# Performance work log

Measured on AMD Instinct MI355X. Metric: run time of the kernel, lower is better.

Reference implementation:

```python
import jax, jax.numpy as jnp
import numpy as np

L = 4      # number of Verifier layers in the linked list
D = 1536   # constraint matrix dimension


def setup_inputs() -> dict:
    key = jax.random.key(0)
    ks = jax.random.split(key, 6)
    scale = 0.02  # keep chained matmul magnitudes sane
    lb = jax.random.normal(ks[0], (1, D), jnp.float32)
    ub = lb + jax.random.uniform(ks[1], (1, D), jnp.float32)  # ensure lb <= ub
    lcs = scale * jax.random.normal(ks[2], (L, D, D), jnp.float32)
    ucs = lcs + scale * jax.random.uniform(ks[3], (L, D, D), jnp.float32)
    lc_bias = jax.random.normal(ks[4], (L, D), jnp.float32)
    uc_bias = lc_bias + jax.random.uniform(ks[5], (L, D), jnp.float32)
    return {"lb": lb, "ub": ub, "lcs": lcs, "ucs": ucs,
            "lc_bias": lc_bias, "uc_bias": uc_bias}


def reference(lb, ub, lcs, ucs, lc_bias, uc_bias):
    pos = lambda x: jnp.maximum(x, 0.0)
    neg = lambda x: jnp.minimum(x, 0.0)
    n_layers = lcs.shape[0]

    # Layer 0 forward: its backsubstitution returns these bounds unchanged
    # (prev is None), and all later backsubs terminate on these stored bounds.
    lb0 = lb @ pos(lcs[0]).T + ub @ neg(lcs[0]).T + lc_bias[0]
    ub0 = ub @ pos(ucs[0]).T + lb @ neg(ucs[0]).T + uc_bias[0]
    cur_lb, cur_ub = lb0, ub0

    for k in range(1, n_layers):
        # backsubstitution from layer k: start with transposed constraint
        C_lc, C_uc = lcs[k].T, ucs[k].T           # [D, D]
        C_lcb, C_ucb = lc_bias[k], uc_bias[k]     # [D]
        # recurse through layers k-1 .. 0, combining constraints
        for j in range(k - 1, -1, -1):
            pU, nU = pos(C_uc), neg(C_uc)
            pL, nL = pos(C_lc), neg(C_lc)
            new_ucb = uc_bias[j] @ pU + lc_bias[j] @ nU + C_ucb
            new_uc = ucs[j].T @ pU + lcs[j].T @ nU
            new_lcb = lc_bias[j] @ pL + uc_bias[j] @ nL + C_lcb
            new_lc = lcs[j].T @ pL + ucs[j].T @ nL
            C_lc, C_uc, C_lcb, C_ucb = new_lc, new_uc, new_lcb, new_ucb
        # apply combined constraint to layer-0 stored bounds
        cur_lb = lb0 @ pos(C_lc) + ub0 @ neg(C_lc) + C_lcb
        cur_ub = ub0 @ pos(C_uc) + lb0 @ neg(C_uc) + C_ucb

    return cur_lb, cur_ub
```

## Files before the change

### kernel.cpp

```cpp
#include <hip/hip_runtime.h>

#define D 1536
#define BT 96
#define BK 64
#define NT (D / BK)
#define TT 64

typedef unsigned short u16;
typedef short bf16x8 __attribute__((ext_vector_type(8)));
typedef short short2v __attribute__((ext_vector_type(2)));
typedef float f32x4 __attribute__((ext_vector_type(4)));

static __device__ __forceinline__ float bf2f(u16 s) {
    unsigned u = ((unsigned)s) << 16;
    float f; __builtin_memcpy(&f, &u, 4); return f;
}
static __device__ __forceinline__ u16 f2bf(float f) {
    unsigned u; __builtin_memcpy(&u, &f, 4);
    unsigned r = (u + 0x7FFFu + ((u >> 16) & 1u)) >> 16;
    return (u16)r;
}

static __device__ __forceinline__ void splitpn(bf16x8 a, bf16x8& p, bf16x8& n) {
    union U { bf16x8 v; short2v s[4]; unsigned u[4]; } x, up, un;
    x.v = a;
#pragma unroll
    for (int i = 0; i < 4; ++i) {
        short2v m = x.s[i] >> 15;
        unsigned mu; __builtin_memcpy(&mu, &m, 4);
        unsigned ng = x.u[i] & mu;
        un.u[i] = ng;
        up.u[i] = x.u[i] ^ ng;
    }
    p = up.v; n = un.v;
}

#define GLDS(g, s) __builtin_amdgcn_global_load_lds( \
    (const __attribute__((address_space(1))) void*)(g), \
    (__attribute__((address_space(3))) void*)(s), 16, 0, 0)

__global__ __launch_bounds__(256) void prep_k(
    const float* __restrict__ lcs, const float* __restrict__ ucs,
    u16* __restrict__ lcsT, u16* __restrict__ ucsT,
    u16* __restrict__ Ga, u16* __restrict__ Gc)
{
    const int z = blockIdx.z;
    const int r0 = blockIdx.y * TT, c0 = blockIdx.x * TT;
    const int tid = threadIdx.x;

    if (z >= 6) {
        const float* src = (z == 6 ? ucs : lcs) + (size_t)3 * D * D;
        u16* dst = (z == 6) ? Ga : Gc;
#pragma unroll
        for (int i = 0; i < 2; ++i) {
            int r = (tid >> 3) + i * 32, cc = (tid & 7) * 8;
            const float* p = src + (size_t)(r0 + r) * D + c0 + cc;
            f32x4 x0 = *(const f32x4*)p;
            f32x4 x1 = *(const f32x4*)(p + 4);
            bf16x8 y;
#pragma unroll
            for (int e = 0; e < 4; ++e) { y[e] = (short)f2bf(x0[e]); y[e + 4] = (short)f2bf(x1[e]); }
            *(bf16x8*)(dst + (size_t)(r0 + r) * D + c0 + cc) = y;
        }
        return;
    }

    __shared__ u16 t[TT][TT + 8];
    const int j = z >> 1, sel = z & 1;
    const float* src = (sel ? ucs : lcs) + (size_t)j * D * D;
    u16* dst = (sel ? ucsT : lcsT) + (size_t)j * D * D;
#pragma unroll
    for (int i = 0; i < 2; ++i) {
        int c = tid + i * 256; int r = c >> 3, v = c & 7;
        const float* p = src + (size_t)(r0 + r) * D + c0 + v * 8;
        f32x4 x0 = *(const f32x4*)p;
        f32x4 x1 = *(const f32x4*)(p + 4);
        bf16x8 y;
#pragma unroll
        for (int e = 0; e < 4; ++e) { y[e] = (short)f2bf(x0[e]); y[e + 4] = (short)f2bf(x1[e]); }
        *(bf16x8*)&t[r][v * 8] = y;
    }
    __syncthreads();
#pragma unroll
    for (int i = 0; i < 2; ++i) {
        int c = tid + i * 256; int rr = c >> 3, v = c & 7;
        bf16x8 x;
#pragma unroll
        for (int e = 0; e < 8; ++e) x[e] = (short)t[v * 8 + e][rr];
        *(bf16x8*)(dst + (size_t)(c0 + rr) * D + r0 + v * 8) = x;
    }
}

__global__ __launch_bounds__(256) void vec_k(
    const float* __restrict__ lb, const float* __restrict__ ub,
    const float* __restrict__ lcs, const float* __restrict__ ucs,
    const float* __restrict__ lcb, const float* __restrict__ ucb,
    float* __restrict__ lb0, float* __restrict__ ub0,
    float* __restrict__ cb_uc, float* __restrict__ cb_lc)
{
    const int tt = blockIdx.x * 4 + (threadIdx.x >> 6);
    const int lane = threadIdx.x & 63;
    const int kind = tt >> 10;
    const int n = tt & 1535;
    const int which = tt / D;
    const int row_n = tt - which * D;

    const float* row; const float* vp; const float* vn;
    if (which == 0)      { row = lcs + (size_t)row_n * D;               vp = lb;           vn = ub; }
    else if (which == 1) { row = ucs + (size_t)row_n * D;               vp = ub;           vn = lb; }
    else if (which == 2) { row = ucs + (size_t)(3 * (size_t)D * D) + (size_t)row_n * D; vp = ucb + 2 * D; vn = lcb + 2 * D; }
    else                 { row = lcs + (size_t)(3 * (size_t)D * D) + (size_t)row_n * D; vp = lcb + 2 * D; vn = ucb + 2 * D; }

    float s = 0.f;
    for (int c2 = 0; c2 < D / 256; ++c2) {
        int base = (c2 * 64 + lane) * 4;
        f32x4 g = *(const f32x4*)(row + base);
        f32x4 p = *(const f32x4*)(vp + base);
        f32x4 m = *(const f32x4*)(vn + base);
#pragma unroll
        for (int e = 0; e < 4; ++e) s += g[e] * (g[e] > 0.f ? p[e] : m[e]);
    }
#pragma unroll
    for (int o = 32; o; o >>= 1) s += __shfl_down(s, o);
    if (lane == 0) {
        if (which == 0)      lb0[row_n] = s + lcb[row_n];
        else if (which == 1) ub0[row_n] = s + ucb[row_n];
        else if (which == 2) cb_uc[row_n] = s + ucb[3 * D + row_n];
        else                 cb_lc[row_n] = s + lcb[3 * D + row_n];
    }
    (void)kind; (void)n;
}

struct GemmArgs { };

static __device__ __forceinline__ void stage_tile(
    const u16* __restrict__ A, const u16* __restrict__ Bp, const u16* __restrict__ Bn,
    int r0, int c0, int kt, u16* __restrict__ sbuf, int tid, int wid)
{
#pragma unroll
    for (int i = 0; i < 9; ++i) {
        const int idx = (i % 3) * 256 + tid;
        const int row = idx >> 3;
        const int kc = tid & 7;
        const int kcg = kc ^ (row & 7);
        const u16* base = (i < 3) ? (A + (size_t)(r0 + row) * D)
                        : ((i < 6) ? (Bp + (size_t)(c0 + row) * D)
                                   : (Bn + (size_t)(c0 + row) * D));
        GLDS(base + kt + kcg * 8, (char*)sbuf + (i * 256 + wid * 64) * 16);
    }
}

static __device__ __forceinline__ void compute_tile(
    const u16* __restrict__ sbuf, f32x4 (&acc)[3][3], int mb, int nb, int lrow, int lk)
{
#pragma unroll
    for (int ks = 0; ks < 2; ++ks) {
        const int slot = ks * 4 + lk;
        bf16x8 pa[3], na[3];
#pragma unroll
        for (int mi = 0; mi < 3; ++mi) {
            int row = mb + mi * 16 + lrow;
            int x = slot ^ (row & 7);
            bf16x8 a = *(const bf16x8*)(sbuf + row * BK + x * 8);
            splitpn(a, pa[mi], na[mi]);
        }
#pragma unroll
        for (int ni = 0; ni < 3; ++ni) {
            int row = nb + ni * 16 + lrow;
            int x = slot ^ (row & 7);
            bf16x8 bu = *(const bf16x8*)(sbuf + BT * BK + row * BK + x * 8);
            bf16x8 bl = *(const bf16x8*)(sbuf + 2 * BT * BK + row * BK + x * 8);
#pragma unroll
            for (int mi = 0; mi < 3; ++mi) {
                acc[mi][ni] = __builtin_amdgcn_mfma_f32_16x16x32_bf16(pa[mi], bu, acc[mi][ni], 0, 0, 0);
                acc[mi][ni] = __builtin_amdgcn_mfma_f32_16x16x32_bf16(na[mi], bl, acc[mi][ni], 0, 0, 0);
            }
        }
    }
}

__global__ __launch_bounds__(256, 2) void gemm_step(
    const u16* __restrict__ Guc, const u16* __restrict__ Glc,
    const u16* __restrict__ lcsTj, const u16* __restrict__ ucsTj,
    u16* __restrict__ outU, u16* __restrict__ outL,
    const float* __restrict__ ucbN, const float* __restrict__ lcbN,
    float* __restrict__ cb_uc, float* __restrict__ cb_lc)
{
    __shared__ u16 smemA[3 * BT * BK];
    __shared__ u16 smemB[3 * BT * BK];
    const int chain = blockIdx.z;
    const u16* A  = chain ? Glc : Guc;
    const u16* Bp = chain ? lcsTj : ucsTj;
    const u16* Bn = chain ? ucsTj : lcsTj;
    u16* out = chain ? outL : outU;
    const int r0 = blockIdx.y * BT, c0 = blockIdx.x * BT;
    const int tid = threadIdx.x, lane = tid & 63, wid = tid >> 6;
    const int mb = (wid >> 1) * 48, nb = (wid & 1) * 48;
    const int lrow = lane & 15, lk = lane >> 4;

    f32x4 acc[3][3] = {};

    stage_tile(A, Bp, Bn, r0, c0, 0, smemA, tid, wid);
    asm volatile("s_waitcnt vmcnt(0)" ::: "memory");
    __syncthreads();

#pragma unroll 1
    for (int t2 = 0; t2 < NT / 2; ++t2) {
        const int t = t2 * 2;
        stage_tile(A, Bp, Bn, r0, c0, (t + 1) * BK, smemB, tid, wid);
        compute_tile(smemA, acc, mb, nb, lrow, lk);
        __syncthreads();
        if (t2 < NT / 2 - 1)
            stage_tile(A, Bp, Bn, r0, c0, (t + 2) * BK, smemA, tid, wid);
        compute_tile(smemB, acc, mb, nb, lrow, lk);
        __syncthreads();
    }

    if (ucbN) {
        const float* pb_ = chain ? lcbN : ucbN;
        const float* nb_ = chain ? ucbN : lcbN;
        float* cb = chain ? cb_lc : cb_uc;
        float pbv[3], nbv[3];
#pragma unroll
        for (int ni = 0; ni < 3; ++ni) {
            int c = c0 + nb + ni * 16 + lrow;
            pbv[ni] = pb_[c]; nbv[ni] = nb_[c];
        }
#pragma unroll
        for (int mi = 0; mi < 3; ++mi)
#pragma unroll
            for (int q = 0; q < 4; ++q) {
                float s = 0.f;
#pragma unroll
                for (int ni = 0; ni < 3; ++ni) {
                    float g = acc[mi][ni][q];
                    s += g * (g > 0.f ? pbv[ni] : nbv[ni]);
                }
                s += __shfl_xor(s, 1); s += __shfl_xor(s, 2);
                s += __shfl_xor(s, 4); s += __shfl_xor(s, 8);
                if (lrow == 0)
                    atomicAdd(&cb[r0 + mb + mi * 16 + lk * 4 + q], s);
            }
    }

#pragma unroll
    for (int mi = 0; mi < 3; ++mi)
#pragma unroll
        for (int ni = 0; ni < 3; ++ni) {
            int c = c0 + nb + ni * 16 + lrow;
            int rbase = r0 + mb + mi * 16 + lk * 4;
#pragma unroll
            for (int q = 0; q < 4; ++q)
                out[(size_t)(rbase + q) * D + c] = f2bf(acc[mi][ni][q]);
        }
}

__global__ __launch_bounds__(256) void final_k(
    const u16* __restrict__ Guc, const u16* __restrict__ Glc,
    const float* __restrict__ cb_uc, const float* __restrict__ cb_lc,
    const float* __restrict__ lb0, const float* __restrict__ ub0,
    float* __restrict__ out)
{
    const int gw = blockIdx.x * 4 + (threadIdx.x >> 6);
    const int lane = threadIdx.x & 63;
    const int which = gw >= D;
    const int n = which ? gw - D : gw;
    const u16* row = (which ? Guc : Glc) + (size_t)n * D;
    const float* vp = which ? ub0 : lb0;
    const float* vn = which ? lb0 : ub0;
    float s = 0.f;
    for (int c2 = 0; c2 < D / 512; ++c2) {
        int base = (c2 * 64 + lane) * 8;
        bf16x8 g8 = *(const bf16x8*)(row + base);
        f32x4 p0 = *(const f32x4*)(vp + base);
        f32x4 p1 = *(const f32x4*)(vp + base + 4);
        f32x4 n0 = *(const f32x4*)(vn + base);
        f32x4 n1 = *(const f32x4*)(vn + base + 4);
#pragma unroll
        for (int e = 0; e < 8; ++e) {
            float g = bf2f((u16)g8[e]);
            float pv = e < 4 ? p0[e] : p1[e - 4];
            float nv = e < 4 ? n0[e] : n1[e - 4];
            s += g * (g > 0.f ? pv : nv);
        }
    }
#pragma unroll
    for (int o = 32; o; o >>= 1) s += __shfl_down(s, o);
    if (lane == 0) {
        float b = (which ? cb_uc : cb_lc)[n];
        out[which * D + n] = s + b;
    }
}

extern "C" void kernel_launch(void* const* d_in, const int* in_sizes, int n_in,
                              void* d_out, int out_size, void* d_ws, size_t ws_size,
                              hipStream_t stream) {
    const float* lb  = (const float*)d_in[0];
    const float* ub  = (const float*)d_in[1];
    const float* lcs = (const float*)d_in[2];
    const float* ucs = (const float*)d_in[3];
    const float* lcb = (const float*)d_in[4];
    const float* ucb = (const float*)d_in[5];
    float* out = (float*)d_out;

    const size_t DD = (size_t)D * D;
    u16* ws   = (u16*)d_ws;
    u16* lcsT = ws;
    u16* ucsT = lcsT + 3 * DD;
    u16* Ga = ucsT + 3 * DD;
    u16* Gb = Ga + DD;
    u16* Gc = Gb + DD;
    u16* Gd = Gc + DD;
    float* fbuf  = (float*)(Gd + DD);
    float* lb0   = fbuf;
    float* ub0   = fbuf + D;
    float* cb_uc = fbuf + 2 * D;
    float* cb_lc = fbuf + 3 * D;

    prep_k<<<dim3(D / TT, D / TT, 8), 256, 0, stream>>>(lcs, ucs, lcsT, ucsT, Ga, Gc);
    vec_k<<<dim3(4 * D / 4), 256, 0, stream>>>(lb, ub, lcs, ucs, lcb, ucb, lb0, ub0, cb_uc, cb_lc);

    u16* curU = Ga; u16* curL = Gc;
    u16* altU = Gb; u16* altL = Gd;
    for (int j = 2; j >= 0; --j) {
        const float* ucbN = (j > 0) ? (ucb + (size_t)(j - 1) * D) : nullptr;
        const float* lcbN = (j > 0) ? (lcb + (size_t)(j - 1) * D) : nullptr;
        gemm_step<<<dim3(D / BT, D / BT, 2), 256, 0, stream>>>(
            curU, curL, lcsT + (size_t)j * DD, ucsT + (size_t)j * DD, altU, altL,
            ucbN, lcbN, cb_uc, cb_lc);
        u16* t;
        t = curU; curU = altU; altU = t;
        t = curL; curL = altL; altL = t;
    }
    final_k<<<dim3(2 * D / 4), 256, 0, stream>>>(curU, curL, cb_uc, cb_lc, lb0, ub0, out);
}
```

Baseline: 134.2 us.

## Fuse upper/lower chains in one GEMM block with triple-buffered LDS pipeline

Each block now computes both the upper and lower constraint chains for the same output tile, so the B tiles (ucsT, lcsT) are loaded once and shared by both chains instead of once per chain via blockIdx.z. The k-loop changes from double buffering to a three-stage ring with explicit vmcnt waits and raw barriers, prefetching two tiles ahead. The cost is half as many blocks (256 instead of 512), twice the accumulators per thread and 144 KB of LDS with occupancy dropped to one block per CU, which may leave some CUs idle or underutilised.

```diff
diff --git a/kernel.cpp b/kernel.cpp
--- a/kernel.cpp
+++ b/kernel.cpp
@@ -5,6 +5,8 @@
 #define BK 64
 #define NT (D / BK)
 #define TT 64
+#define TILE_E (BT * BK)
+#define BUF_E (4 * TILE_E)
 
 typedef unsigned short u16;
 typedef short bf16x8 __attribute__((ext_vector_type(8)));
@@ -39,6 +41,8 @@
     (const __attribute__((address_space(1))) void*)(g), \
     (__attribute__((address_space(3))) void*)(s), 16, 0, 0)
 
+#define MFMA16(a, b, c) __builtin_amdgcn_mfma_f32_16x16x32_bf16(a, b, c, 0, 0, 0)
+
 __global__ __launch_bounds__(256) void prep_k(
     const float* __restrict__ lcs, const float* __restrict__ ucs,
     u16* __restrict__ lcsT, u16* __restrict__ ucsT,
@@ -100,8 +104,6 @@
 {
     const int tt = blockIdx.x * 4 + (threadIdx.x >> 6);
     const int lane = threadIdx.x & 63;
-    const int kind = tt >> 10;
-    const int n = tt & 1535;
     const int which = tt / D;
     const int row_n = tt - which * D;
 
@@ -128,118 +130,126 @@
         else if (which == 2) cb_uc[row_n] = s + ucb[3 * D + row_n];
         else                 cb_lc[row_n] = s + lcb[3 * D + row_n];
     }
-    (void)kind; (void)n;
-}
-
-struct GemmArgs { };
+}
+
 
 static __device__ __forceinline__ void stage_tile(
-    const u16* __restrict__ A, const u16* __restrict__ Bp, const u16* __restrict__ Bn,
+    const u16* __restrict__ Au, const u16* __restrict__ Al,
+    const u16* __restrict__ Bu, const u16* __restrict__ Bl,
     int r0, int c0, int kt, u16* __restrict__ sbuf, int tid, int wid)
 {
 #pragma unroll
-    for (int i = 0; i < 9; ++i) {
+    for (int i = 0; i < 12; ++i) {
         const int idx = (i % 3) * 256 + tid;
         const int row = idx >> 3;
-        const int kc = tid & 7;
-        const int kcg = kc ^ (row & 7);
-        const u16* base = (i < 3) ? (A + (size_t)(r0 + row) * D)
-                        : ((i < 6) ? (Bp + (size_t)(c0 + row) * D)
-                                   : (Bn + (size_t)(c0 + row) * D));
-        GLDS(base + kt + kcg * 8, (char*)sbuf + (i * 256 + wid * 64) * 16);
+        const int kcg = (tid & 7) ^ (row & 7);
+        const u16* base; int ro;
+        if (i < 3)      { base = Au; ro = r0; }
+        else if (i < 6) { base = Al; ro = r0; }
+        else if (i < 9) { base = Bu; ro = c0; }
+        else            { base = Bl; ro = c0; }
+        GLDS(base + (size_t)(ro + row) * D + kt + kcg * 8,
+             (char*)sbuf + (i * 256 + wid * 64) * 16);
     }
 }
 
 static __device__ __forceinline__ void compute_tile(
-    const u16* __restrict__ sbuf, f32x4 (&acc)[3][3], int mb, int nb, int lrow, int lk)
+    const u16* __restrict__ sbuf, f32x4 (&accU)[3][3], f32x4 (&accL)[3][3],
+    int mb, int nb, int lrow, int lk)
 {
 #pragma unroll
     for (int ks = 0; ks < 2; ++ks) {
         const int slot = ks * 4 + lk;
-        bf16x8 pa[3], na[3];
+        bf16x8 pu[3], nu[3], pl[3], nl[3];
 #pragma unroll
         for (int mi = 0; mi < 3; ++mi) {
             int row = mb + mi * 16 + lrow;
             int x = slot ^ (row & 7);
-            bf16x8 a = *(const bf16x8*)(sbuf + row * BK + x * 8);
-            splitpn(a, pa[mi], na[mi]);
+            bf16x8 au = *(const bf16x8*)(sbuf + row * BK + x * 8);
+            bf16x8 al = *(const bf16x8*)(sbuf + TILE_E + row * BK + x * 8);
+            splitpn(au, pu[mi], nu[mi]);
+            splitpn(al, pl[mi], nl[mi]);
         }
 #pragma unroll
         for (int ni = 0; ni < 3; ++ni) {
             int row = nb + ni * 16 + lrow;
             int x = slot ^ (row & 7);
-            bf16x8 bu = *(const bf16x8*)(sbuf + BT * BK + row * BK + x * 8);
-            bf16x8 bl = *(const bf16x8*)(sbuf + 2 * BT * BK + row * BK + x * 8);
+            bf16x8 bu = *(const bf16x8*)(sbuf + 2 * TILE_E + row * BK + x * 8);
+            bf16x8 bl = *(const bf16x8*)(sbuf + 3 * TILE_E + row * BK + x * 8);
 #pragma unroll
             for (int mi = 0; mi < 3; ++mi) {
-                acc[mi][ni] = __builtin_amdgcn_mfma_f32_16x16x32_bf16(pa[mi], bu, acc[mi][ni], 0, 0, 0);
-                acc[mi][ni] = __builtin_amdgcn_mfma_f32_16x16x32_bf16(na[mi], bl, acc[mi][ni], 0, 0, 0);
+                accU[mi][ni] = MFMA16(pu[mi], bu, accU[mi][ni]);
+                accU[mi][ni] = MFMA16(nu[mi], bl, accU[mi][ni]);
+                accL[mi][ni] = MFMA16(pl[mi], bl, accL[mi][ni]);
+                accL[mi][ni] = MFMA16(nl[mi], bu, accL[mi][ni]);
             }
         }
     }
 }
 
-__global__ __launch_bounds__(256, 2) void gemm_step(
+__global__ __launch_bounds__(256, 1) void gemm_step(
     const u16* __restrict__ Guc, const u16* __restrict__ Glc,
     const u16* __restrict__ lcsTj, const u16* __restrict__ ucsTj,
     u16* __restrict__ outU, u16* __restrict__ outL,
     const float* __restrict__ ucbN, const float* __restrict__ lcbN,
     float* __restrict__ cb_uc, float* __restrict__ cb_lc)
 {
-    __shared__ u16 smemA[3 * BT * BK];
-    __shared__ u16 smemB[3 * BT * BK];
-    const int chain = blockIdx.z;
-    const u16* A  = chain ? Glc : Guc;
-    const u16* Bp = chain ? lcsTj : ucsTj;
-    const u16* Bn = chain ? ucsTj : lcsTj;
-    u16* out = chain ? outL : outU;
+    __shared__ u16 smem[3 * BUF_E];
     const int r0 = blockIdx.y * BT, c0 = blockIdx.x * BT;
     const int tid = threadIdx.x, lane = tid & 63, wid = tid >> 6;
     const int mb = (wid >> 1) * 48, nb = (wid & 1) * 48;
     const int lrow = lane & 15, lk = lane >> 4;
 
-    f32x4 acc[3][3] = {};
-
-    stage_tile(A, Bp, Bn, r0, c0, 0, smemA, tid, wid);
-    asm volatile("s_waitcnt vmcnt(0)" ::: "memory");
-    __syncthreads();
+    f32x4 accU[3][3] = {}, accL[3][3] = {};
+
+    stage_tile(Guc, Glc, ucsTj, lcsTj, r0, c0, 0, smem, tid, wid);
+    stage_tile(Guc, Glc, ucsTj, lcsTj, r0, c0, BK, smem + BUF_E, tid, wid);
 
 #pragma unroll 1
-    for (int t2 = 0; t2 < NT / 2; ++t2) {
-        const int t = t2 * 2;
-        stage_tile(A, Bp, Bn, r0, c0, (t + 1) * BK, smemB, tid, wid);
-        compute_tile(smemA, acc, mb, nb, lrow, lk);
-        __syncthreads();
-        if (t2 < NT / 2 - 1)
-            stage_tile(A, Bp, Bn, r0, c0, (t + 2) * BK, smemA, tid, wid);
-        compute_tile(smemB, acc, mb, nb, lrow, lk);
-        __syncthreads();
+    for (int t = 0; t < NT; ++t) {
+        if (t + 2 < NT) {
+            stage_tile(Guc, Glc, ucsTj, lcsTj, r0, c0, (t + 2) * BK,
+                       smem + ((t + 2) % 3) * BUF_E, tid, wid);
+            asm volatile("s_waitcnt vmcnt(24)" ::: "memory");
+        } else if (t + 2 == NT) {
+            asm volatile("s_waitcnt vmcnt(12)" ::: "memory");
+        } else {
+            asm volatile("s_waitcnt vmcnt(0)" ::: "memory");
+        }
+        __builtin_amdgcn_s_barrier();
+        compute_tile(smem + (t % 3) * BUF_E, accU, accL, mb, nb, lrow, lk);
+        asm volatile("" ::: "memory");
+        __builtin_amdgcn_s_barrier();
     }
 
     if (ucbN) {
-        const float* pb_ = chain ? lcbN : ucbN;
-        const float* nb_ = chain ? ucbN : lcbN;
-        float* cb = chain ? cb_lc : cb_uc;
-        float pbv[3], nbv[3];
+        float ubv[3], lbv[3];
 #pragma unroll
         for (int ni = 0; ni < 3; ++ni) {
             int c = c0 + nb + ni * 16 + lrow;
-            pbv[ni] = pb_[c]; nbv[ni] = nb_[c];
+            ubv[ni] = ucbN[c]; lbv[ni] = lcbN[c];
         }
 #pragma unroll
         for (int mi = 0; mi < 3; ++mi)
 #pragma unroll
             for (int q = 0; q < 4; ++q) {
-                float s = 0.f;
+                float sU = 0.f, sL = 0.f;
 #pragma unroll
                 for (int ni = 0; ni < 3; ++ni) {
-                    float g = acc[mi][ni][q];
-                    s += g * (g > 0.f ? pbv[ni] : nbv[ni]);
+                    float gU = accU[mi][ni][q];
+                    float gL = accL[mi][ni][q];
+                    sU += gU * (gU > 0.f ? ubv[ni] : lbv[ni]);
+                    sL += gL * (gL > 0.f ? lbv[ni] : ubv[ni]);
                 }
-                s += __shfl_xor(s, 1); s += __shfl_xor(s, 2);
-                s += __shfl_xor(s, 4); s += __shfl_xor(s, 8);
-                if (lrow == 0)
-                    atomicAdd(&cb[r0 + mb + mi * 16 + lk * 4 + q], s);
+                sU += __shfl_xor(sU, 1); sU += __shfl_xor(sU, 2);
+                sU += __shfl_xor(sU, 4); sU += __shfl_xor(sU, 8);
+                sL += __shfl_xor(sL, 1); sL += __shfl_xor(sL, 2);
+                sL += __shfl_xor(sL, 4); sL += __shfl_xor(sL, 8);
+                if (lrow == 0) {
+                    int r = r0 + mb + mi * 16 + lk * 4 + q;
+                    atomicAdd(&cb_uc[r], sU);
+                    atomicAdd(&cb_lc[r], sL);
+                }
             }
     }
 
@@ -250,8 +260,10 @@
             int c = c0 + nb + ni * 16 + lrow;
             int rbase = r0 + mb + mi * 16 + lk * 4;
 #pragma unroll
-            for (int q = 0; q < 4; ++q)
-                out[(size_t)(rbase + q) * D + c] = f2bf(acc[mi][ni][q]);
+            for (int q = 0; q < 4; ++q) {
+                outU[(size_t)(rbase + q) * D + c] = f2bf(accU[mi][ni][q]);
+                outL[(size_t)(rbase + q) * D + c] = f2bf(accL[mi][ni][q]);
+            }
         }
 }
 
@@ -325,7 +337,7 @@
     for (int j = 2; j >= 0; --j) {
         const float* ucbN = (j > 0) ? (ucb + (size_t)(j - 1) * D) : nullptr;
         const float* lcbN = (j > 0) ? (lcb + (size_t)(j - 1) * D) : nullptr;
-        gemm_step<<<dim3(D / BT, D / BT, 2), 256, 0, stream>>>(
+        gemm_step<<<dim3(D / BT, D / BT), 256, 0, stream>>>(
             curU, curL, lcsT + (size_t)j * DD, ucsT + (size_t)j * DD, altU, altL,
             ucbN, lcbN, cb_uc, cb_lc);
         u16* t;
```

Result: slower. 155.1 us (+15.6%).

## Use sum/difference B matrices with abs-sign A operand and deeper GEMM pipelining

Applied to the files above, without the earlier changes.

Replaces the positive/negative split of the A operand with an algebraic identity. The transposed ucs/lcs are preprocessed into half-sum and half-difference matrices, so each MFMA pair uses A as-is and |A| (sign-flipped for the lower chain) instead of masking into pos/neg parts. This cuts per-tile VALU splitting work and folds the chain-dependent B swap into a sign constant. The GEMM loop is also restructured to keep two tiles in flight with partial vmcnt waits and raw s_barrier, which aims for better overlap of loads and compute. The bf16 rounding of the (u±l)/2 values may change numerics slightly.

```diff
diff --git a/kernel.cpp b/kernel.cpp
--- a/kernel.cpp
+++ b/kernel.cpp
@@ -5,89 +5,91 @@
 #define BK 64
 #define NT (D / BK)
 #define TT 64
+#define TILE_E (BT * BK)
+#define BUF_E (3 * TILE_E)
 
 typedef unsigned short u16;
 typedef short bf16x8 __attribute__((ext_vector_type(8)));
-typedef short short2v __attribute__((ext_vector_type(2)));
 typedef float f32x4 __attribute__((ext_vector_type(4)));
 
-static __device__ __forceinline__ float bf2f(u16 s) {
-    unsigned u = ((unsigned)s) << 16;
-    float f; __builtin_memcpy(&f, &u, 4); return f;
-}
 static __device__ __forceinline__ u16 f2bf(float f) {
     unsigned u; __builtin_memcpy(&u, &f, 4);
     unsigned r = (u + 0x7FFFu + ((u >> 16) & 1u)) >> 16;
     return (u16)r;
 }
-
-static __device__ __forceinline__ void splitpn(bf16x8 a, bf16x8& p, bf16x8& n) {
-    union U { bf16x8 v; short2v s[4]; unsigned u[4]; } x, up, un;
-    x.v = a;
-#pragma unroll
-    for (int i = 0; i < 4; ++i) {
-        short2v m = x.s[i] >> 15;
-        unsigned mu; __builtin_memcpy(&mu, &m, 4);
-        unsigned ng = x.u[i] & mu;
-        un.u[i] = ng;
-        up.u[i] = x.u[i] ^ ng;
-    }
-    p = up.v; n = un.v;
+static __device__ __forceinline__ float bf2f(u16 s) {
+    unsigned u = ((unsigned)s) << 16;
+    float f; __builtin_memcpy(&f, &u, 4); return f;
 }
 
 #define GLDS(g, s) __builtin_amdgcn_global_load_lds( \
     (const __attribute__((address_space(1))) void*)(g), \
     (__attribute__((address_space(3))) void*)(s), 16, 0, 0)
 
+#define MFMA16(a, b, c) __builtin_amdgcn_mfma_f32_16x16x32_bf16(a, b, c, 0, 0, 0)
+
 __global__ __launch_bounds__(256) void prep_k(
     const float* __restrict__ lcs, const float* __restrict__ ucs,
-    u16* __restrict__ lcsT, u16* __restrict__ ucsT,
+    u16* __restrict__ BsT, u16* __restrict__ BdT,
     u16* __restrict__ Ga, u16* __restrict__ Gc)
 {
     const int z = blockIdx.z;
     const int r0 = blockIdx.y * TT, c0 = blockIdx.x * TT;
     const int tid = threadIdx.x;
 
-    if (z >= 6) {
-        const float* src = (z == 6 ? ucs : lcs) + (size_t)3 * D * D;
-        u16* dst = (z == 6) ? Ga : Gc;
-#pragma unroll
-        for (int i = 0; i < 2; ++i) {
-            int r = (tid >> 3) + i * 32, cc = (tid & 7) * 8;
-            const float* p = src + (size_t)(r0 + r) * D + c0 + cc;
-            f32x4 x0 = *(const f32x4*)p;
-            f32x4 x1 = *(const f32x4*)(p + 4);
-            bf16x8 y;
-#pragma unroll
-            for (int e = 0; e < 4; ++e) { y[e] = (short)f2bf(x0[e]); y[e + 4] = (short)f2bf(x1[e]); }
-            *(bf16x8*)(dst + (size_t)(r0 + r) * D + c0 + cc) = y;
+    if (z == 3) {
+#pragma unroll
+        for (int m = 0; m < 2; ++m) {
+            const float* src = (m ? lcs : ucs) + (size_t)3 * D * D;
+            u16* dst = m ? Gc : Ga;
+#pragma unroll
+            for (int i = 0; i < 2; ++i) {
+                int r = (tid >> 3) + i * 32, cc = (tid & 7) * 8;
+                const float* p = src + (size_t)(r0 + r) * D + c0 + cc;
+                f32x4 x0 = *(const f32x4*)p;
+                f32x4 x1 = *(const f32x4*)(p + 4);
+                bf16x8 y;
+#pragma unroll
+                for (int e = 0; e < 4; ++e) { y[e] = (short)f2bf(x0[e]); y[e + 4] = (short)f2bf(x1[e]); }
+                *(bf16x8*)(dst + (size_t)(r0 + r) * D + c0 + cc) = y;
+            }
         }
         return;
     }
 
-    __shared__ u16 t[TT][TT + 8];
-    const int j = z >> 1, sel = z & 1;
-    const float* src = (sel ? ucs : lcs) + (size_t)j * D * D;
-    u16* dst = (sel ? ucsT : lcsT) + (size_t)j * D * D;
+    __shared__ u16 ts[TT][TT + 8];
+    __shared__ u16 td[TT][TT + 8];
+    const float* srcl = lcs + (size_t)z * D * D;
+    const float* srcu = ucs + (size_t)z * D * D;
 #pragma unroll
     for (int i = 0; i < 2; ++i) {
         int c = tid + i * 256; int r = c >> 3, v = c & 7;
-        const float* p = src + (size_t)(r0 + r) * D + c0 + v * 8;
-        f32x4 x0 = *(const f32x4*)p;
-        f32x4 x1 = *(const f32x4*)(p + 4);
-        bf16x8 y;
-#pragma unroll
-        for (int e = 0; e < 4; ++e) { y[e] = (short)f2bf(x0[e]); y[e + 4] = (short)f2bf(x1[e]); }
-        *(bf16x8*)&t[r][v * 8] = y;
+        size_t off = (size_t)(r0 + r) * D + c0 + v * 8;
+        f32x4 l0 = *(const f32x4*)(srcl + off);
+        f32x4 l1 = *(const f32x4*)(srcl + off + 4);
+        f32x4 u0 = *(const f32x4*)(srcu + off);
+        f32x4 u1 = *(const f32x4*)(srcu + off + 4);
+        bf16x8 ys, yd;
+#pragma unroll
+        for (int e = 0; e < 4; ++e) {
+            ys[e]     = (short)f2bf((u0[e] + l0[e]) * 0.5f);
+            yd[e]     = (short)f2bf((u0[e] - l0[e]) * 0.5f);
+            ys[e + 4] = (short)f2bf((u1[e] + l1[e]) * 0.5f);
+            yd[e + 4] = (short)f2bf((u1[e] - l1[e]) * 0.5f);
+        }
+        *(bf16x8*)&ts[r][v * 8] = ys;
+        *(bf16x8*)&td[r][v * 8] = yd;
     }
     __syncthreads();
 #pragma unroll
     for (int i = 0; i < 2; ++i) {
         int c = tid + i * 256; int rr = c >> 3, v = c & 7;
-        bf16x8 x;
-#pragma unroll
-        for (int e = 0; e < 8; ++e) x[e] = (short)t[v * 8 + e][rr];
-        *(bf16x8*)(dst + (size_t)(c0 + rr) * D + r0 + v * 8) = x;
+        bf16x8 xs, xd;
+#pragma unroll
+        for (int e = 0; e < 8; ++e) { xs[e] = (short)ts[v * 8 + e][rr]; xd[e] = (short)td[v * 8 + e][rr]; }
+        size_t off = (size_t)z * D * D + (size_t)(c0 + rr) * D + r0 + v * 8;
+        *(bf16x8*)(BsT + off) = xs;
+        *(bf16x8*)(BdT + off) = xd;
     }
 }
 
@@ -100,8 +102,6 @@
 {
     const int tt = blockIdx.x * 4 + (threadIdx.x >> 6);
     const int lane = threadIdx.x & 63;
-    const int kind = tt >> 10;
-    const int n = tt & 1535;
     const int which = tt / D;
     const int row_n = tt - which * D;
 
@@ -128,52 +128,54 @@
         else if (which == 2) cb_uc[row_n] = s + ucb[3 * D + row_n];
         else                 cb_lc[row_n] = s + lcb[3 * D + row_n];
     }
-    (void)kind; (void)n;
-}
-
-struct GemmArgs { };
+}
+
 
 static __device__ __forceinline__ void stage_tile(
-    const u16* __restrict__ A, const u16* __restrict__ Bp, const u16* __restrict__ Bn,
+    const u16* __restrict__ A, const u16* __restrict__ Bs, const u16* __restrict__ Bd,
     int r0, int c0, int kt, u16* __restrict__ sbuf, int tid, int wid)
 {
 #pragma unroll
     for (int i = 0; i < 9; ++i) {
         const int idx = (i % 3) * 256 + tid;
         const int row = idx >> 3;
-        const int kc = tid & 7;
-        const int kcg = kc ^ (row & 7);
+        const int kcg = (tid & 7) ^ (row & 7);
         const u16* base = (i < 3) ? (A + (size_t)(r0 + row) * D)
-                        : ((i < 6) ? (Bp + (size_t)(c0 + row) * D)
-                                   : (Bn + (size_t)(c0 + row) * D));
+                        : ((i < 6) ? (Bs + (size_t)(c0 + row) * D)
+                                   : (Bd + (size_t)(c0 + row) * D));
         GLDS(base + kt + kcg * 8, (char*)sbuf + (i * 256 + wid * 64) * 16);
     }
 }
 
 static __device__ __forceinline__ void compute_tile(
-    const u16* __restrict__ sbuf, f32x4 (&acc)[3][3], int mb, int nb, int lrow, int lk)
+    const u16* __restrict__ sbuf, f32x4 (&acc)[3][3], unsigned sgn,
+    int mb, int nb, int lrow, int lk)
 {
 #pragma unroll
     for (int ks = 0; ks < 2; ++ks) {
         const int slot = ks * 4 + lk;
-        bf16x8 pa[3], na[3];
+        bf16x8 a[3], x[3];
 #pragma unroll
         for (int mi = 0; mi < 3; ++mi) {
             int row = mb + mi * 16 + lrow;
-            int x = slot ^ (row & 7);
-            bf16x8 a = *(const bf16x8*)(sbuf + row * BK + x * 8);
-            splitpn(a, pa[mi], na[mi]);
+            int xx = slot ^ (row & 7);
+            a[mi] = *(const bf16x8*)(sbuf + row * BK + xx * 8);
+            union { bf16x8 v; unsigned u[4]; } t, o;
+            t.v = a[mi];
+#pragma unroll
+            for (int q = 0; q < 4; ++q) o.u[q] = (t.u[q] & 0x7FFF7FFFu) ^ sgn;
+            x[mi] = o.v;
         }
 #pragma unroll
         for (int ni = 0; ni < 3; ++ni) {
             int row = nb + ni * 16 + lrow;
-            int x = slot ^ (row & 7);
-            bf16x8 bu = *(const bf16x8*)(sbuf + BT * BK + row * BK + x * 8);
-            bf16x8 bl = *(const bf16x8*)(sbuf + 2 * BT * BK + row * BK + x * 8);
+            int xx = slot ^ (row & 7);
+            bf16x8 bs = *(const bf16x8*)(sbuf + TILE_E + row * BK + xx * 8);
+            bf16x8 bd = *(const bf16x8*)(sbuf + 2 * TILE_E + row * BK + xx * 8);
 #pragma unroll
             for (int mi = 0; mi < 3; ++mi) {
-                acc[mi][ni] = __builtin_amdgcn_mfma_f32_16x16x32_bf16(pa[mi], bu, acc[mi][ni], 0, 0, 0);
-                acc[mi][ni] = __builtin_amdgcn_mfma_f32_16x16x32_bf16(na[mi], bl, acc[mi][ni], 0, 0, 0);
+                acc[mi][ni] = MFMA16(a[mi], bs, acc[mi][ni]);
+                acc[mi][ni] = MFMA16(x[mi], bd, acc[mi][ni]);
             }
         }
     }
@@ -181,18 +183,16 @@
 
 __global__ __launch_bounds__(256, 2) void gemm_step(
     const u16* __restrict__ Guc, const u16* __restrict__ Glc,
-    const u16* __restrict__ lcsTj, const u16* __restrict__ ucsTj,
+    const u16* __restrict__ Bs, const u16* __restrict__ Bd,
     u16* __restrict__ outU, u16* __restrict__ outL,
     const float* __restrict__ ucbN, const float* __restrict__ lcbN,
     float* __restrict__ cb_uc, float* __restrict__ cb_lc)
 {
-    __shared__ u16 smemA[3 * BT * BK];
-    __shared__ u16 smemB[3 * BT * BK];
+    __shared__ u16 smem[2 * BUF_E];
     const int chain = blockIdx.z;
-    const u16* A  = chain ? Glc : Guc;
-    const u16* Bp = chain ? lcsTj : ucsTj;
-    const u16* Bn = chain ? ucsTj : lcsTj;
+    const u16* A = chain ? Glc : Guc;
     u16* out = chain ? outL : outU;
+    const unsigned sgn = chain ? 0x80008000u : 0u;
     const int r0 = blockIdx.y * BT, c0 = blockIdx.x * BT;
     const int tid = threadIdx.x, lane = tid & 63, wid = tid >> 6;
     const int mb = (wid >> 1) * 48, nb = (wid & 1) * 48;
@@ -200,20 +200,19 @@
 
     f32x4 acc[3][3] = {};
 
-    stage_tile(A, Bp, Bn, r0, c0, 0, smemA, tid, wid);
-    asm volatile("s_waitcnt vmcnt(0)" ::: "memory");
-    __syncthreads();
+    stage_tile(A, Bs, Bd, r0, c0, 0, smem, tid, wid);
+    stage_tile(A, Bs, Bd, r0, c0, BK, smem + BUF_E, tid, wid);
 
 #pragma unroll 1
-    for (int t2 = 0; t2 < NT / 2; ++t2) {
-        const int t = t2 * 2;
-        stage_tile(A, Bp, Bn, r0, c0, (t + 1) * BK, smemB, tid, wid);
-        compute_tile(smemA, acc, mb, nb, lrow, lk);
-        __syncthreads();
-        if (t2 < NT / 2 - 1)
-            stage_tile(A, Bp, Bn, r0, c0, (t + 2) * BK, smemA, tid, wid);
-        compute_tile(smemB, acc, mb, nb, lrow, lk);
-        __syncthreads();
+    for (int t = 0; t < NT; ++t) {
+        if (t < NT - 1) { asm volatile("s_waitcnt vmcnt(9)" ::: "memory"); }
+        else            { asm volatile("s_waitcnt vmcnt(0)" ::: "memory"); }
+        __builtin_amdgcn_sched_barrier(0);
+        __builtin_amdgcn_s_barrier();
+        compute_tile(smem + (t & 1) * BUF_E, acc, sgn, mb, nb, lrow, lk);
+        __builtin_amdgcn_s_barrier();
+        if (t + 2 < NT)
+            stage_tile(A, Bs, Bd, r0, c0, (t + 2) * BK, smem + (t & 1) * BUF_E, tid, wid);
     }
 
     if (ucbN) {
@@ -305,9 +304,9 @@
 
     const size_t DD = (size_t)D * D;
     u16* ws   = (u16*)d_ws;
-    u16* lcsT = ws;
-    u16* ucsT = lcsT + 3 * DD;
-    u16* Ga = ucsT + 3 * DD;
+    u16* BsT = ws;
+    u16* BdT = BsT + 3 * DD;
+    u16* Ga = BdT + 3 * DD;
     u16* Gb = Ga + DD;
     u16* Gc = Gb + DD;
     u16* Gd = Gc + DD;
@@ -317,7 +316,7 @@
     float* cb_uc = fbuf + 2 * D;
     float* cb_lc = fbuf + 3 * D;
 
-    prep_k<<<dim3(D / TT, D / TT, 8), 256, 0, stream>>>(lcs, ucs, lcsT, ucsT, Ga, Gc);
+    prep_k<<<dim3(D / TT, D / TT, 4), 256, 0, stream>>>(lcs, ucs, BsT, BdT, Ga, Gc);
     vec_k<<<dim3(4 * D / 4), 256, 0, stream>>>(lb, ub, lcs, ucs, lcb, ucb, lb0, ub0, cb_uc, cb_lc);
 
     u16* curU = Ga; u16* curL = Gc;
@@ -326,7 +325,7 @@
         const float* ucbN = (j > 0) ? (ucb + (size_t)(j - 1) * D) : nullptr;
         const float* lcbN = (j > 0) ? (lcb + (size_t)(j - 1) * D) : nullptr;
         gemm_step<<<dim3(D / BT, D / BT, 2), 256, 0, stream>>>(
-            curU, curL, lcsT + (size_t)j * DD, ucsT + (size_t)j * DD, altU, altL,
+            curU, curL, BsT + (size_t)j * DD, BdT + (size_t)j * DD, altU, altL,
             ucbN, lcbN, cb_uc, cb_lc);
         u16* t;
         t = curU; curU = altU; altU = t;
```

Result: faster. 128.2 us (-4.5%).
